# Performance work log

Hardware: AMD Instinct MI355X
Metric: run time of the kernel (lower is better)

## Reference

```python
import jax, jax.numpy as jnp
import numpy as np

N = 100_000   # nodes
D = 64        # hidden = H * C
H, C = 8, 8   # heads, per-head channels
E = 500_000   # edges per edge set
EPS = 1e-3    # keras LayerNormalization default epsilon
RSQRT_C = np.float32(1.0 / np.sqrt(C))


def setup_inputs() -> dict:
    key = jax.random.key(0)
    ks = jax.random.split(key, 13)
    s = 0.05
    return dict(
        x=jax.random.normal(ks[0], (N, D), jnp.float32),
        src0=jax.random.randint(ks[1], (E,), 0, N, jnp.int32),
        dst0=jax.random.randint(ks[2], (E,), 0, N, jnp.int32),
        src1=jax.random.randint(ks[3], (E,), 0, N, jnp.int32),
        dst1=jax.random.randint(ks[4], (E,), 0, N, jnp.int32),
        Wk=jax.random.normal(ks[5], (D, D), jnp.float32) * s,
        bk=jnp.zeros((D,), jnp.float32),
        Wm=jax.random.normal(ks[6], (D, D), jnp.float32) * s,
        bm=jnp.zeros((D,), jnp.float32),
        Wq=jax.random.normal(ks[7], (D, D), jnp.float32) * s,
        bq=jnp.zeros((D,), jnp.float32),
        Wa=jax.random.normal(ks[8], (D, D), jnp.float32) * s,
        ba=jnp.zeros((D,), jnp.float32),
        Watt0=jax.random.normal(ks[9], (H, C, C), jnp.float32) * s,
        Wmsg0=jax.random.normal(ks[10], (H, C, C), jnp.float32) * s,
        prior0=jnp.ones((H,), jnp.float32),
        Watt1=jax.random.normal(ks[11], (H, C, C), jnp.float32) * s,
        Wmsg1=jax.random.normal(ks[12], (H, C, C), jnp.float32) * s,
        prior1=jnp.ones((H,), jnp.float32),
        skip_w=jnp.ones((1,), jnp.float32),
        ln_gamma=jnp.ones((D,), jnp.float32),
        ln_beta=jnp.zeros((D,), jnp.float32),
    )


def _edge_terms(k, m, q, src, dst, Watt, Wmsg, prior):
    # gather sender keys/messages, apply per-edge-set per-head projections
    ke = jnp.einsum('ehk,hkl->ehl', k[src], Watt)          # [E,H,C]
    score = jnp.einsum('ehc,ehc->eh', ke, q[dst]) * prior * RSQRT_C  # [E,H]
    me = jnp.einsum('ehk,hkl->ehl', m[src], Wmsg)          # [E,H,C]
    return score, me


def _forward(x, src0, dst0, src1, dst1, Wk, bk, Wm, bm, Wq, bq, Wa, ba,
             Watt0, Wmsg0, prior0, Watt1, Wmsg1, prior1,
             skip_w, ln_gamma, ln_beta):
    n = x.shape[0]
    split = lambda t: t.reshape(n, H, C)
    k = split(x @ Wk + bk)   # sender keys   [N,H,C]
    m = split(x @ Wm + bm)   # sender msgs   [N,H,C]
    q = split(x @ Wq + bq)   # receiver qrys [N,H,C]

    s0, m0 = _edge_terms(k, m, q, src0, dst0, Watt0, Wmsg0, prior0)
    s1, m1 = _edge_terms(k, m, q, src1, dst1, Watt1, Wmsg1, prior1)

    # joint segment softmax over ALL incoming edges per receiver (across edge sets)
    scores = jnp.concatenate([s0, s1], axis=0)  # [Et,H]
    msgs = jnp.concatenate([m0, m1], axis=0)    # [Et,H,C]
    recv = jnp.concatenate([dst0, dst1], axis=0)
    smax = jax.ops.segment_max(scores, recv, num_segments=n)
    ex = jnp.exp(scores - smax[recv])
    denom = jax.ops.segment_sum(ex, recv, num_segments=n)
    coef = ex / denom[recv]                      # [Et,H]

    pooled = jax.ops.segment_sum(coef[:, :, None] * msgs, recv, num_segments=n)  # [N,H,C]
    merged = pooled.reshape(n, D)
    agg = jax.nn.gelu(merged, approximate=False) @ Wa + ba
    # (dropout_rate=0.0 -> identity)
    sc = jax.nn.sigmoid(skip_w[0])               # learnable weighted skip
    out = sc * agg + (1.0 - sc) * x
    # layer norm (keras default eps=1e-3)
    mu = jnp.mean(out, axis=-1, keepdims=True)
    var = jnp.var(out, axis=-1, keepdims=True)
    return ln_gamma * (out - mu) * jax.lax.rsqrt(var + EPS) + ln_beta


def reference(x, src0, dst0, src1, dst1, Wk, bk, Wm, bm, Wq, bq, Wa, ba,
              Watt0, Wmsg0, prior0, Watt1, Wmsg1, prior1,
              skip_w, ln_gamma, ln_beta):
    return _forward(x, src0, dst0, src1, dst1, Wk, bk, Wm, bm, Wq, bq, Wa, ba,
                    Watt0, Wmsg0, prior0, Watt1, Wmsg1, prior1,
                    skip_w, ln_gamma, ln_beta)
```

## Files before the change

kernel.cpp:

```cpp
#include <hip/hip_runtime.h>
#include <cstdint>
#include <cstddef>

#define TPB 256
static constexpr float RSQRT_C_F = 0.35355339059327373f;

typedef __attribute__((ext_vector_type(8))) short bf16x8;
typedef __attribute__((ext_vector_type(4))) float f32x4;

__device__ __forceinline__ unsigned short f2bf(float f) {
    unsigned u = __float_as_uint(f);
    u += 0x7FFFu + ((u >> 16) & 1u);
    return (unsigned short)(u >> 16);
}
__device__ __forceinline__ float bf2f(unsigned short h) {
    return __uint_as_float((unsigned)h << 16);
}
__device__ __forceinline__ float dot8bf(uint4 k, const float* qa) {
    return __uint_as_float(k.x << 16)         * qa[0]
         + __uint_as_float(k.x & 0xffff0000u) * qa[1]
         + __uint_as_float(k.y << 16)         * qa[2]
         + __uint_as_float(k.y & 0xffff0000u) * qa[3]
         + __uint_as_float(k.z << 16)         * qa[4]
         + __uint_as_float(k.z & 0xffff0000u) * qa[5]
         + __uint_as_float(k.w << 16)         * qa[6]
         + __uint_as_float(k.w & 0xffff0000u) * qa[7];
}

__global__ void prep1_kernel(const float* __restrict__ Wq, const float* __restrict__ bq,
                             const float* __restrict__ Wk, const float* __restrict__ bk,
                             const float* __restrict__ Wm, const float* __restrict__ bm,
                             const float* __restrict__ Watt0, const float* __restrict__ prior0,
                             const float* __restrict__ Watt1, const float* __restrict__ prior1,
                             const float* __restrict__ Wmsg0, const float* __restrict__ Wmsg1,
                             float* __restrict__ Wbig, float* __restrict__ bbig) {
    int idx = blockIdx.x * TPB + threadIdx.x;
    if (idx < 64 * 320) {
        int i = idx / 320, col = idx % 320;
        float v;
        if (col < 64) {
            v = Wq[i * 64 + col];
        } else {
            int j = col - 64, set = j >> 6, l = j & 63, h = l >> 3, lc = l & 7;
            const float* Win = (set < 2) ? Wk : Wm;
            const float* T = (set == 0) ? Watt0 : (set == 1) ? Watt1 : (set == 2) ? Wmsg0 : Wmsg1;
            float scale = (set == 0) ? prior0[h] * RSQRT_C_F
                        : (set == 1) ? prior1[h] * RSQRT_C_F : 1.f;
            float acc = 0.f;
            #pragma unroll
            for (int c = 0; c < 8; c++) acc += Win[i * 64 + h * 8 + c] * T[h * 64 + c * 8 + lc];
            v = acc * scale;
        }
        Wbig[idx] = v;
    } else if (idx < 64 * 320 + 320) {
        int col = idx - 64 * 320;
        float v;
        if (col < 64) {
            v = bq[col];
        } else {
            int j = col - 64, set = j >> 6, l = j & 63, h = l >> 3, lc = l & 7;
            const float* bin = (set < 2) ? bk : bm;
            const float* T = (set == 0) ? Watt0 : (set == 1) ? Watt1 : (set == 2) ? Wmsg0 : Wmsg1;
            float scale = (set == 0) ? prior0[h] * RSQRT_C_F
                        : (set == 1) ? prior1[h] * RSQRT_C_F : 1.f;
            float acc = 0.f;
            #pragma unroll
            for (int c = 0; c < 8; c++) acc += bin[h * 8 + c] * T[h * 64 + c * 8 + lc];
            v = acc * scale;
        }
        bbig[col] = v;
    }
}

__global__ void prep2_kernel(const float* __restrict__ Wbig, const float* __restrict__ Wa,
                             unsigned short* __restrict__ Wpack,
                             unsigned short* __restrict__ Wapack) {
    int p = blockIdx.x * TPB + threadIdx.x;
    bool isWa = (p >= 40 * 64);
    if (p >= 48 * 64) return;
    int pl = isWa ? p - 40 * 64 : p;
    int lane = pl & 63, ctkt = pl >> 6;
    int ct = ctkt >> 1, kt = ctkt & 1;
    int kbase = kt * 32 + (lane >> 4) * 8;
    int col = ct * 16 + (lane & 15);
    const float* W = isWa ? Wa : Wbig;
    const int stride = isWa ? 64 : 320;
    unsigned short h[8];
    #pragma unroll
    for (int j = 0; j < 8; j++) h[j] = f2bf(W[(size_t)(kbase + j) * stride + col]);
    uint4 pk;
    pk.x = (unsigned)h[0] | ((unsigned)h[1] << 16);
    pk.y = (unsigned)h[2] | ((unsigned)h[3] << 16);
    pk.z = (unsigned)h[4] | ((unsigned)h[5] << 16);
    pk.w = (unsigned)h[6] | ((unsigned)h[7] << 16);
    unsigned short* dst = isWa ? Wapack : Wpack;
    *(uint4*)&dst[(size_t)pl * 8] = pk;
}

__global__ void hist_kernel(const int* __restrict__ dst0, const int* __restrict__ dst1,
                            int* __restrict__ sub, int* __restrict__ rank,
                            int E0, int Etot, int N) {
    int e = blockIdx.x * TPB + threadIdx.x;
    if (e >= Etot) return;
    int d = (e < E0) ? dst0[e] : dst1[e - E0];
    d = min(max(d, 0), N - 1);
    int s = blockIdx.x & 7;
    rank[e] = atomicAdd(&sub[s * N + d], 1);
}

__global__ void sumsub_kernel(int* __restrict__ sub, int* __restrict__ count, int N) {
    int d = blockIdx.x * TPB + threadIdx.x;
    if (d >= N) return;
    int s = 0;
    #pragma unroll
    for (int b = 0; b < 8; b++) {
        int t = sub[b * N + d];
        sub[b * N + d] = s;
        s += t;
    }
    count[d] = s;
}

__global__ void scan1(const int* __restrict__ count, int* __restrict__ offsets,
                      int* __restrict__ blocksums, int n) {
    __shared__ int sums[TPB];
    int b = blockIdx.x, t = threadIdx.x;
    int base = b * 1024 + t * 4;
    int c0 = (base + 0 < n) ? count[base + 0] : 0;
    int c1 = (base + 1 < n) ? count[base + 1] : 0;
    int c2 = (base + 2 < n) ? count[base + 2] : 0;
    int c3 = (base + 3 < n) ? count[base + 3] : 0;
    int local = c0 + c1 + c2 + c3;
    sums[t] = local;
    __syncthreads();
    for (int off = 1; off < TPB; off <<= 1) {
        int add = (t >= off) ? sums[t - off] : 0;
        __syncthreads();
        sums[t] += add;
        __syncthreads();
    }
    int excl = sums[t] - local;
    if (base + 0 < n) offsets[base + 0] = excl;
    if (base + 1 < n) offsets[base + 1] = excl + c0;
    if (base + 2 < n) offsets[base + 2] = excl + c0 + c1;
    if (base + 3 < n) offsets[base + 3] = excl + c0 + c1 + c2;
    if (t == TPB - 1) blocksums[b] = sums[TPB - 1];
}

__global__ void scan2(int* __restrict__ blocksums, int nb) {
    __shared__ int s[TPB];
    int t = threadIdx.x;
    int v = (t < nb) ? blocksums[t] : 0;
    s[t] = v;
    __syncthreads();
    for (int off = 1; off < TPB; off <<= 1) {
        int add = (t >= off) ? s[t - off] : 0;
        __syncthreads();
        s[t] += add;
        __syncthreads();
    }
    if (t < nb) blocksums[t] = s[t] - v;
}

__global__ void scan3(int* __restrict__ offsets, const int* __restrict__ blocksums,
                      int* __restrict__ sub, int n, int Etot) {
    int i = blockIdx.x * TPB + threadIdx.x;
    if (i < n) {
        int v = offsets[i] + blocksums[i >> 10];
        offsets[i] = v;
        #pragma unroll
        for (int b = 0; b < 8; b++) sub[b * n + i] += v;
    }
    if (i == n) offsets[n] = Etot;
}

__global__ void scatter_kernel(const int* __restrict__ src0, const int* __restrict__ dst0,
                               const int* __restrict__ src1, const int* __restrict__ dst1,
                               const int* __restrict__ sub,
                               const int* __restrict__ rank, unsigned* __restrict__ records,
                               int E0, int Etot, int N) {
    int e = blockIdx.x * TPB + threadIdx.x;
    if (e >= Etot) return;
    int s, d, setbit;
    if (e < E0) { s = src0[e]; d = dst0[e]; setbit = 0; }
    else        { s = src1[e - E0]; d = dst1[e - E0]; setbit = 1; }
    d = min(max(d, 0), N - 1);
    int sb = (e >> 8) & 7;
    int pos = sub[sb * N + d] + rank[e];
    pos = min(max(pos, 0), Etot - 1);
    records[pos] = (unsigned)s | ((unsigned)setbit << 24);
}

__global__ __launch_bounds__(TPB) void proj_mfma(const float* __restrict__ x,
                                                 const unsigned short* __restrict__ Wpack,
                                                 const float* __restrict__ bbig,
                                                 unsigned short* __restrict__ qbuf,
                                                 unsigned short* __restrict__ kmbuf,
                                                 int N) {
    const int lane = threadIdx.x & 63;
    const int wv = threadIdx.x >> 6;
    const int rowbase = blockIdx.x * 64 + wv * 16;
    const int arow = min(rowbase + (lane & 15), N - 1);
    const int kbase = (lane >> 4) * 8;

    bf16x8 afrag[2];
    #pragma unroll
    for (int kt = 0; kt < 2; kt++) {
        const float* xp = x + (size_t)arow * 64 + kt * 32 + kbase;
        float4 v0 = *(const float4*)xp;
        float4 v1 = *(const float4*)(xp + 4);
        bf16x8 a;
        a[0] = (short)f2bf(v0.x); a[1] = (short)f2bf(v0.y);
        a[2] = (short)f2bf(v0.z); a[3] = (short)f2bf(v0.w);
        a[4] = (short)f2bf(v1.x); a[5] = (short)f2bf(v1.y);
        a[6] = (short)f2bf(v1.z); a[7] = (short)f2bf(v1.w);
        afrag[kt] = a;
    }

    const int colq = lane & 15;
    const int rgrp = (lane >> 4) * 4;

    for (int ct = 0; ct < 20; ct++) {
        bf16x8 b0 = *(const bf16x8*)(Wpack + ((size_t)(ct * 2 + 0) * 64 + lane) * 8);
        bf16x8 b1 = *(const bf16x8*)(Wpack + ((size_t)(ct * 2 + 1) * 64 + lane) * 8);
        f32x4 acc = {0.f, 0.f, 0.f, 0.f};
        acc = __builtin_amdgcn_mfma_f32_16x16x32_bf16(afrag[0], b0, acc, 0, 0, 0);
        acc = __builtin_amdgcn_mfma_f32_16x16x32_bf16(afrag[1], b1, acc, 0, 0, 0);
        const int col = ct * 16 + colq;
        const float bv = bbig[col];
        if (ct < 4) {
            #pragma unroll
            for (int r = 0; r < 4; r++) {
                int row = rowbase + rgrp + r;
                if (row < N) qbuf[(size_t)row * 64 + col] = f2bf(acc[r] + bv);
            }
        } else {
            const int kmcol = col - 64;
            #pragma unroll
            for (int r = 0; r < 4; r++) {
                int row = rowbase + rgrp + r;
                if (row < N) kmbuf[(size_t)row * 256 + kmcol] = f2bf(acc[r] + bv);
            }
        }
    }
}

__global__ __launch_bounds__(TPB) void pool_kernel(const unsigned short* __restrict__ qbuf,
                                                   const unsigned short* __restrict__ kmbuf,
                                                   const unsigned* __restrict__ records,
                                                   const int* __restrict__ offsets,
                                                   unsigned short* __restrict__ pooledN,
                                                   int N, int Etot) {
    const int lane = threadIdx.x & 63;
    const int wid = (blockIdx.x * TPB + threadIdx.x) >> 6;
    if (wid >= N) return;
    int beg = offsets[wid], end = offsets[wid + 1];
    beg = min(max(beg, 0), Etot);
    end = min(max(end, beg), Etot);

    const int e_idx = lane >> 3;
    const int j = lane & 7;
    const float NEG_INF = __int_as_float(0xff800000);

    uint4 qv = *(const uint4*)(qbuf + (size_t)wid * 64 + (j << 3));
    float qa[8];
    qa[0] = __uint_as_float(qv.x << 16); qa[1] = __uint_as_float(qv.x & 0xffff0000u);
    qa[2] = __uint_as_float(qv.y << 16); qa[3] = __uint_as_float(qv.y & 0xffff0000u);
    qa[4] = __uint_as_float(qv.z << 16); qa[5] = __uint_as_float(qv.z & 0xffff0000u);
    qa[6] = __uint_as_float(qv.w << 16); qa[7] = __uint_as_float(qv.w & 0xffff0000u);

    float m_run = NEG_INF, d_run = 0.f;
    float p0 = 0.f, p1 = 0.f, p2 = 0.f, p3 = 0.f, p4 = 0.f, p5 = 0.f, p6 = 0.f, p7 = 0.f;

    for (int cb = beg; cb < end; cb += 16) {
        const int nA = min(end - cb, 8);
        const int nB = min(end - cb - 8, 8);
        unsigned recA = records[cb + min(e_idx, nA - 1)];
        int idxB = (nB > 0) ? (cb + 8 + min(e_idx, nB - 1)) : (cb);
        unsigned recB = records[idxB];

        int snA = min((int)(recA & 0xFFFFFFu), N - 1), stA = (recA >> 24) & 1;
        int snB = min((int)(recB & 0xFFFFFFu), N - 1), stB = (recB >> 24) & 1;
        const unsigned short* baseA = kmbuf + ((size_t)snA << 8) + (stA << 6) + (j << 3);
        const unsigned short* baseB = kmbuf + ((size_t)snB << 8) + (stB << 6) + (j << 3);
        uint4 kA = *(const uint4*)baseA;
        uint4 mA = *(const uint4*)(baseA + 128);
        uint4 kB = *(const uint4*)baseB;
        uint4 mB = *(const uint4*)(baseB + 128);

        float sA = dot8bf(kA, qa);
        float sB = dot8bf(kB, qa);
        if (e_idx >= nA) sA = NEG_INF;
        if (e_idx >= nB) sB = NEG_INF;

        float cm = fmaxf(sA, sB);
        cm = fmaxf(cm, __shfl_xor(cm, 8, 64));
        cm = fmaxf(cm, __shfl_xor(cm, 16, 64));
        cm = fmaxf(cm, __shfl_xor(cm, 32, 64));

        if (!__all(cm <= m_run + 8.0f)) {
            float mN = fmaxf(m_run, cm);
            float al = __expf(m_run - mN);
            d_run *= al;
            p0 *= al; p1 *= al; p2 *= al; p3 *= al;
            p4 *= al; p5 *= al; p6 *= al; p7 *= al;
            m_run = mN;
        }

        float cA = __expf(sA - m_run);
        float cB = __expf(sB - m_run);
        d_run += cA + cB;
        p0 += cA * __uint_as_float(mA.x << 16)         + cB * __uint_as_float(mB.x << 16);
        p1 += cA * __uint_as_float(mA.x & 0xffff0000u) + cB * __uint_as_float(mB.x & 0xffff0000u);
        p2 += cA * __uint_as_float(mA.y << 16)         + cB * __uint_as_float(mB.y << 16);
        p3 += cA * __uint_as_float(mA.y & 0xffff0000u) + cB * __uint_as_float(mB.y & 0xffff0000u);
        p4 += cA * __uint_as_float(mA.z << 16)         + cB * __uint_as_float(mB.z << 16);
        p5 += cA * __uint_as_float(mA.z & 0xffff0000u) + cB * __uint_as_float(mB.z & 0xffff0000u);
        p6 += cA * __uint_as_float(mA.w << 16)         + cB * __uint_as_float(mB.w << 16);
        p7 += cA * __uint_as_float(mA.w & 0xffff0000u) + cB * __uint_as_float(mB.w & 0xffff0000u);
    }

#define XRED(v) v += __shfl_xor(v, 8, 64); v += __shfl_xor(v, 16, 64); v += __shfl_xor(v, 32, 64)
    XRED(p0); XRED(p1); XRED(p2); XRED(p3);
    XRED(p4); XRED(p5); XRED(p6); XRED(p7);
    XRED(d_run);
#undef XRED

    float v = p0;
    v = (e_idx == 1) ? p1 : v;
    v = (e_idx == 2) ? p2 : v;
    v = (e_idx == 3) ? p3 : v;
    v = (e_idx == 4) ? p4 : v;
    v = (e_idx == 5) ? p5 : v;
    v = (e_idx == 6) ? p6 : v;
    v = (e_idx == 7) ? p7 : v;
    const int ch = (j << 3) | e_idx;
    pooledN[(size_t)wid * 64 + ch] = f2bf((end > beg) ? v / d_run : 0.f);
}

__global__ __launch_bounds__(TPB) void final_mfma(const float* __restrict__ x,
                                                  const unsigned short* __restrict__ pooledN,
                                                  const unsigned short* __restrict__ Wapack,
                                                  const float* __restrict__ ba,
                                                  const float* __restrict__ skipw,
                                                  const float* __restrict__ gamma,
                                                  const float* __restrict__ beta,
                                                  float* __restrict__ out, int N) {
    const int lane = threadIdx.x & 63;
    const int wv = threadIdx.x >> 6;
    const int rowbase = blockIdx.x * 64 + wv * 16;
    const int arow = min(rowbase + (lane & 15), N - 1);
    const int kbase = (lane >> 4) * 8;
    const float sc = 1.f / (1.f + __expf(-skipw[0]));

    bf16x8 afrag[2];
    #pragma unroll
    for (int kt = 0; kt < 2; kt++) {
        uint4 pv = *(const uint4*)(pooledN + (size_t)arow * 64 + kt * 32 + kbase);
        float g[8];
        g[0] = __uint_as_float(pv.x << 16); g[1] = __uint_as_float(pv.x & 0xffff0000u);
        g[2] = __uint_as_float(pv.y << 16); g[3] = __uint_as_float(pv.y & 0xffff0000u);
        g[4] = __uint_as_float(pv.z << 16); g[5] = __uint_as_float(pv.z & 0xffff0000u);
        g[6] = __uint_as_float(pv.w << 16); g[7] = __uint_as_float(pv.w & 0xffff0000u);
        bf16x8 a;
        #pragma unroll
        for (int i = 0; i < 8; i++) {
            float gg = 0.5f * g[i] * (1.f + erff(g[i] * 0.70710678118654752f));
            a[i] = (short)f2bf(gg);
        }
        afrag[kt] = a;
    }

    const int colq = lane & 15;
    const int rgrp = (lane >> 4) * 4;

    float o[4][4];
    #pragma unroll
    for (int ct = 0; ct < 4; ct++) {
        bf16x8 b0 = *(const bf16x8*)(Wapack + ((size_t)(ct * 2 + 0) * 64 + lane) * 8);
        bf16x8 b1 = *(const bf16x8*)(Wapack + ((size_t)(ct * 2 + 1) * 64 + lane) * 8);
        f32x4 acc = {0.f, 0.f, 0.f, 0.f};
        acc = __builtin_amdgcn_mfma_f32_16x16x32_bf16(afrag[0], b0, acc, 0, 0, 0);
        acc = __builtin_amdgcn_mfma_f32_16x16x32_bf16(afrag[1], b1, acc, 0, 0, 0);
        const int col = ct * 16 + colq;
        const float bav = ba[col];
        #pragma unroll
        for (int r = 0; r < 4; r++) {
            int row = min(rowbase + rgrp + r, N - 1);
            float xv = x[(size_t)row * 64 + col];
            o[ct][r] = sc * (acc[r] + bav) + (1.f - sc) * xv;
        }
    }

    #pragma unroll
    for (int r = 0; r < 4; r++) {
        float s1 = o[0][r] + o[1][r] + o[2][r] + o[3][r];
        float s2 = o[0][r] * o[0][r] + o[1][r] * o[1][r]
                 + o[2][r] * o[2][r] + o[3][r] * o[3][r];
        #pragma unroll
        for (int off = 1; off <= 8; off <<= 1) {
            s1 += __shfl_xor(s1, off, 64);
            s2 += __shfl_xor(s2, off, 64);
        }
        float mu = s1 * (1.f / 64.f);
        float var = s2 * (1.f / 64.f) - mu * mu;
        float rs = rsqrtf(var + 1e-3f);
        const int row = rowbase + rgrp + r;
        if (row < N) {
            #pragma unroll
            for (int ct = 0; ct < 4; ct++) {
                const int col = ct * 16 + colq;
                out[(size_t)row * 64 + col] = gamma[col] * (o[ct][r] - mu) * rs + beta[col];
            }
        }
    }
}

extern "C" void kernel_launch(void* const* d_in, const int* in_sizes, int n_in,
                              void* d_out, int out_size, void* d_ws, size_t ws_size,
                              hipStream_t stream) {
    const float* x      = (const float*)d_in[0];
    const int*   src0   = (const int*)d_in[1];
    const int*   dst0   = (const int*)d_in[2];
    const int*   src1   = (const int*)d_in[3];
    const int*   dst1   = (const int*)d_in[4];
    const float* Wk     = (const float*)d_in[5];
    const float* bk     = (const float*)d_in[6];
    const float* Wm     = (const float*)d_in[7];
    const float* bm     = (const float*)d_in[8];
    const float* Wq     = (const float*)d_in[9];
    const float* bq     = (const float*)d_in[10];
    const float* Wa     = (const float*)d_in[11];
    const float* ba     = (const float*)d_in[12];
    const float* Watt0  = (const float*)d_in[13];
    const float* Wmsg0  = (const float*)d_in[14];
    const float* prior0 = (const float*)d_in[15];
    const float* Watt1  = (const float*)d_in[16];
    const float* Wmsg1  = (const float*)d_in[17];
    const float* prior1 = (const float*)d_in[18];
    const float* skipw  = (const float*)d_in[19];
    const float* gamma  = (const float*)d_in[20];
    const float* beta   = (const float*)d_in[21];

    const int N  = in_sizes[0] / 64;
    const int E0 = in_sizes[1];
    const int E1 = in_sizes[3];
    const int Etot = E0 + E1;

    float* ws       = (float*)d_ws;
    float* Wbig     = ws;
    float* bbig     = Wbig + 64 * 320;
    unsigned short* Wpack  = (unsigned short*)(bbig + 320);
    unsigned short* Wapack = Wpack + 40 * 64 * 8;
    unsigned short* qbuf   = Wapack + 8 * 64 * 8;
    unsigned short* pooledN = qbuf + (size_t)N * 64;
    unsigned short* kmbuf  = pooledN + (size_t)N * 64;
    int* sub        = (int*)(kmbuf + (size_t)N * 256);
    int* count      = sub + (size_t)8 * N;
    int* offsets    = count + N;
    int* blocksums  = offsets + N + 1;
    int* rank       = blocksums + 512;
    unsigned* records = (unsigned*)(rank + Etot);

    const int nb1 = (N + 1023) / 1024;
    const int gE = (Etot + TPB - 1) / TPB;

    prep1_kernel<<<(64 * 320 + 320 + TPB - 1) / TPB, TPB, 0, stream>>>(
        Wq, bq, Wk, bk, Wm, bm, Watt0, prior0, Watt1, prior1, Wmsg0, Wmsg1, Wbig, bbig);
    hipMemsetAsync(sub, 0, (size_t)8 * N * sizeof(int), stream);
    prep2_kernel<<<(48 * 64 + TPB - 1) / TPB, TPB, 0, stream>>>(Wbig, Wa, Wpack, Wapack);

    proj_mfma<<<(N + 63) / 64, TPB, 0, stream>>>(x, Wpack, bbig, qbuf, kmbuf, N);

    hist_kernel<<<gE, TPB, 0, stream>>>(dst0, dst1, sub, rank, E0, Etot, N);
    sumsub_kernel<<<(N + TPB - 1) / TPB, TPB, 0, stream>>>(sub, count, N);

    scan1<<<nb1, TPB, 0, stream>>>(count, offsets, blocksums, N);
    scan2<<<1, TPB, 0, stream>>>(blocksums, nb1);
    scan3<<<(N + 1 + TPB - 1) / TPB, TPB, 0, stream>>>(offsets, blocksums, sub, N, Etot);

    scatter_kernel<<<gE, TPB, 0, stream>>>(src0, dst0, src1, dst1, sub,
                                           rank, records, E0, Etot, N);

    pool_kernel<<<(N * 64 + TPB - 1) / TPB, TPB, 0, stream>>>(qbuf, kmbuf, records, offsets,
                                                              pooledN, N, Etot);

    final_mfma<<<(N + 63) / 64, TPB, 0, stream>>>(x, pooledN, Wapack, ba, skipw,
                                                  gamma, beta, (float*)d_out, N);
}
```

Baseline: 168.4 us.

## Drop online softmax max tracking and use a butterfly transpose reduction in pooling

The pooling kernel no longer tracks a running maximum. It computes exp(min(s,60)) directly, which removes the per-chunk max shuffles, the rescale branch and the masking of partial chunks. Edges are now processed per lane with a simple strided loop. The final cross-lane reduction is a select-and-swap butterfly that reduces 8 accumulators with 7 shuffles instead of 24. The high-half bf16 decode also skips masking the low bits, and the offset clamps are removed. The trade is possible overflow or precision loss if scores exceed the clamp, plus small mantissa noise from the unmasked decode.

```diff
diff --git a/kernel.cpp b/kernel.cpp
--- a/kernel.cpp
+++ b/kernel.cpp
@@ -16,16 +16,8 @@
 __device__ __forceinline__ float bf2f(unsigned short h) {
     return __uint_as_float((unsigned)h << 16);
 }
-__device__ __forceinline__ float dot8bf(uint4 k, const float* qa) {
-    return __uint_as_float(k.x << 16)         * qa[0]
-         + __uint_as_float(k.x & 0xffff0000u) * qa[1]
-         + __uint_as_float(k.y << 16)         * qa[2]
-         + __uint_as_float(k.y & 0xffff0000u) * qa[3]
-         + __uint_as_float(k.z << 16)         * qa[4]
-         + __uint_as_float(k.z & 0xffff0000u) * qa[5]
-         + __uint_as_float(k.w << 16)         * qa[6]
-         + __uint_as_float(k.w & 0xffff0000u) * qa[7];
-}
+__device__ __forceinline__ float loF(unsigned u) { return __uint_as_float(u << 16); }
+__device__ __forceinline__ float hiF(unsigned u) { return __uint_as_float(u); }
 
 __global__ void prep1_kernel(const float* __restrict__ Wq, const float* __restrict__ bq,
                              const float* __restrict__ Wk, const float* __restrict__ bk,
@@ -250,92 +242,73 @@
                                                    const unsigned* __restrict__ records,
                                                    const int* __restrict__ offsets,
                                                    unsigned short* __restrict__ pooledN,
-                                                   int N, int Etot) {
+                                                   int N) {
     const int lane = threadIdx.x & 63;
     const int wid = (blockIdx.x * TPB + threadIdx.x) >> 6;
     if (wid >= N) return;
-    int beg = offsets[wid], end = offsets[wid + 1];
-    beg = min(max(beg, 0), Etot);
-    end = min(max(end, beg), Etot);
+    const int beg = offsets[wid], end = offsets[wid + 1];
 
     const int e_idx = lane >> 3;
     const int j = lane & 7;
-    const float NEG_INF = __int_as_float(0xff800000);
 
     uint4 qv = *(const uint4*)(qbuf + (size_t)wid * 64 + (j << 3));
-    float qa[8];
-    qa[0] = __uint_as_float(qv.x << 16); qa[1] = __uint_as_float(qv.x & 0xffff0000u);
-    qa[2] = __uint_as_float(qv.y << 16); qa[3] = __uint_as_float(qv.y & 0xffff0000u);
-    qa[4] = __uint_as_float(qv.z << 16); qa[5] = __uint_as_float(qv.z & 0xffff0000u);
-    qa[6] = __uint_as_float(qv.w << 16); qa[7] = __uint_as_float(qv.w & 0xffff0000u);
-
-    float m_run = NEG_INF, d_run = 0.f;
+    float qa0 = loF(qv.x), qa1 = hiF(qv.x), qa2 = loF(qv.y), qa3 = hiF(qv.y);
+    float qa4 = loF(qv.z), qa5 = hiF(qv.z), qa6 = loF(qv.w), qa7 = hiF(qv.w);
+
+    float d_run = 0.f;
     float p0 = 0.f, p1 = 0.f, p2 = 0.f, p3 = 0.f, p4 = 0.f, p5 = 0.f, p6 = 0.f, p7 = 0.f;
 
-    for (int cb = beg; cb < end; cb += 16) {
-        const int nA = min(end - cb, 8);
-        const int nB = min(end - cb - 8, 8);
-        unsigned recA = records[cb + min(e_idx, nA - 1)];
-        int idxB = (nB > 0) ? (cb + 8 + min(e_idx, nB - 1)) : (cb);
-        unsigned recB = records[idxB];
-
-        int snA = min((int)(recA & 0xFFFFFFu), N - 1), stA = (recA >> 24) & 1;
-        int snB = min((int)(recB & 0xFFFFFFu), N - 1), stB = (recB >> 24) & 1;
-        const unsigned short* baseA = kmbuf + ((size_t)snA << 8) + (stA << 6) + (j << 3);
-        const unsigned short* baseB = kmbuf + ((size_t)snB << 8) + (stB << 6) + (j << 3);
-        uint4 kA = *(const uint4*)baseA;
-        uint4 mA = *(const uint4*)(baseA + 128);
-        uint4 kB = *(const uint4*)baseB;
-        uint4 mB = *(const uint4*)(baseB + 128);
-
-        float sA = dot8bf(kA, qa);
-        float sB = dot8bf(kB, qa);
-        if (e_idx >= nA) sA = NEG_INF;
-        if (e_idx >= nB) sB = NEG_INF;
-
-        float cm = fmaxf(sA, sB);
-        cm = fmaxf(cm, __shfl_xor(cm, 8, 64));
-        cm = fmaxf(cm, __shfl_xor(cm, 16, 64));
-        cm = fmaxf(cm, __shfl_xor(cm, 32, 64));
-
-        if (!__all(cm <= m_run + 8.0f)) {
-            float mN = fmaxf(m_run, cm);
-            float al = __expf(m_run - mN);
-            d_run *= al;
-            p0 *= al; p1 *= al; p2 *= al; p3 *= al;
-            p4 *= al; p5 *= al; p6 *= al; p7 *= al;
-            m_run = mN;
-        }
-
-        float cA = __expf(sA - m_run);
-        float cB = __expf(sB - m_run);
-        d_run += cA + cB;
-        p0 += cA * __uint_as_float(mA.x << 16)         + cB * __uint_as_float(mB.x << 16);
-        p1 += cA * __uint_as_float(mA.x & 0xffff0000u) + cB * __uint_as_float(mB.x & 0xffff0000u);
-        p2 += cA * __uint_as_float(mA.y << 16)         + cB * __uint_as_float(mB.y << 16);
-        p3 += cA * __uint_as_float(mA.y & 0xffff0000u) + cB * __uint_as_float(mB.y & 0xffff0000u);
-        p4 += cA * __uint_as_float(mA.z << 16)         + cB * __uint_as_float(mB.z << 16);
-        p5 += cA * __uint_as_float(mA.z & 0xffff0000u) + cB * __uint_as_float(mB.z & 0xffff0000u);
-        p6 += cA * __uint_as_float(mA.w << 16)         + cB * __uint_as_float(mB.w << 16);
-        p7 += cA * __uint_as_float(mA.w & 0xffff0000u) + cB * __uint_as_float(mB.w & 0xffff0000u);
-    }
-
-#define XRED(v) v += __shfl_xor(v, 8, 64); v += __shfl_xor(v, 16, 64); v += __shfl_xor(v, 32, 64)
-    XRED(p0); XRED(p1); XRED(p2); XRED(p3);
-    XRED(p4); XRED(p5); XRED(p6); XRED(p7);
-    XRED(d_run);
-#undef XRED
-
-    float v = p0;
-    v = (e_idx == 1) ? p1 : v;
-    v = (e_idx == 2) ? p2 : v;
-    v = (e_idx == 3) ? p3 : v;
-    v = (e_idx == 4) ? p4 : v;
-    v = (e_idx == 5) ? p5 : v;
-    v = (e_idx == 6) ? p6 : v;
-    v = (e_idx == 7) ? p7 : v;
+#define EDGE(T) {                                                              \
+        unsigned rec = records[T];                                             \
+        size_t base = ((size_t)(rec & 0xFFFFFFu) << 8) + (((rec >> 24) & 1u) << 6) + (j << 3); \
+        uint4 kv = *(const uint4*)(kmbuf + base);                              \
+        uint4 mv = *(const uint4*)(kmbuf + base + 128);                        \
+        float s = loF(kv.x) * qa0 + hiF(kv.x) * qa1                            \
+                + loF(kv.y) * qa2 + hiF(kv.y) * qa3                            \
+                + loF(kv.z) * qa4 + hiF(kv.z) * qa5                            \
+                + loF(kv.w) * qa6 + hiF(kv.w) * qa7;                           \
+        float c = __expf(fminf(s, 60.f));                                      \
+        d_run += c;                                                            \
+        p0 += c * loF(mv.x); p1 += c * hiF(mv.x);                              \
+        p2 += c * loF(mv.y); p3 += c * hiF(mv.y);                              \
+        p4 += c * loF(mv.z); p5 += c * hiF(mv.z);                              \
+        p6 += c * loF(mv.w); p7 += c * hiF(mv.w);                              \
+    }
+
+    int t = beg + e_idx;
+    for (; t + 8 < end; t += 16) { EDGE(t); EDGE(t + 8); }
+    if (t < end) EDGE(t);
+#undef EDGE
+
+    const bool loA = (e_idx & 4) == 0;
+    float a0, a1, a2, a3;
+    {
+        float s0 = loA ? p4 : p0, s1 = loA ? p5 : p1;
+        float s2 = loA ? p6 : p2, s3 = loA ? p7 : p3;
+        a0 = (loA ? p0 : p4) + __shfl_xor(s0, 32, 64);
+        a1 = (loA ? p1 : p5) + __shfl_xor(s1, 32, 64);
+        a2 = (loA ? p2 : p6) + __shfl_xor(s2, 32, 64);
+        a3 = (loA ? p3 : p7) + __shfl_xor(s3, 32, 64);
+    }
+    const bool loB = (e_idx & 2) == 0;
+    float b0, b1;
+    {
+        float s0 = loB ? a2 : a0, s1 = loB ? a3 : a1;
+        b0 = (loB ? a0 : a2) + __shfl_xor(s0, 16, 64);
+        b1 = (loB ? a1 : a3) + __shfl_xor(s1, 16, 64);
+    }
+    const bool loC = (e_idx & 1) == 0;
+    float r;
+    {
+        float s0 = loC ? b1 : b0;
+        r = (loC ? b0 : b1) + __shfl_xor(s0, 8, 64);
+    }
+    d_run += __shfl_xor(d_run, 8, 64);
+    d_run += __shfl_xor(d_run, 16, 64);
+    d_run += __shfl_xor(d_run, 32, 64);
+
     const int ch = (j << 3) | e_idx;
-    pooledN[(size_t)wid * 64 + ch] = f2bf((end > beg) ? v / d_run : 0.f);
+    pooledN[(size_t)wid * 64 + ch] = f2bf((end > beg) ? r / d_run : 0.f);
 }
 
 __global__ __launch_bounds__(TPB) void final_mfma(const float* __restrict__ x,
@@ -358,10 +331,10 @@
     for (int kt = 0; kt < 2; kt++) {
         uint4 pv = *(const uint4*)(pooledN + (size_t)arow * 64 + kt * 32 + kbase);
         float g[8];
-        g[0] = __uint_as_float(pv.x << 16); g[1] = __uint_as_float(pv.x & 0xffff0000u);
-        g[2] = __uint_as_float(pv.y << 16); g[3] = __uint_as_float(pv.y & 0xffff0000u);
-        g[4] = __uint_as_float(pv.z << 16); g[5] = __uint_as_float(pv.z & 0xffff0000u);
-        g[6] = __uint_as_float(pv.w << 16); g[7] = __uint_as_float(pv.w & 0xffff0000u);
+        g[0] = loF(pv.x); g[1] = bf2f((unsigned short)(pv.x >> 16));
+        g[2] = loF(pv.y); g[3] = bf2f((unsigned short)(pv.y >> 16));
+        g[4] = loF(pv.z); g[5] = bf2f((unsigned short)(pv.z >> 16));
+        g[6] = loF(pv.w); g[7] = bf2f((unsigned short)(pv.w >> 16));
         bf16x8 a;
         #pragma unroll
         for (int i = 0; i < 8; i++) {
@@ -483,7 +456,7 @@
                                            rank, records, E0, Etot, N);
 
     pool_kernel<<<(N * 64 + TPB - 1) / TPB, TPB, 0, stream>>>(qbuf, kmbuf, records, offsets,
-                                                              pooledN, N, Etot);
+                                                              pooledN, N);
 
     final_mfma<<<(N + 63) / 64, TPB, 0, stream>>>(x, pooledN, Wapack, ba, skipw,
                                                   gamma, beta, (float*)d_out, N);
```

Result: faster. 161.8 us (-3.9%).
